# Kernel optimization log

Measured on AMD Instinct MI355X. Metric: run time of the kernel, lower is better.

Reference implementation:

```python
import jax, jax.numpy as jnp
import numpy as np

B, J, E, H = 32, 512, 512, 8
HD = E // H
EPS = 1e-7


def log_map0_spatial(x):
    # Lorentz log map at origin o=(1,0,...,0); return spatial (tangent) part.
    x0 = jnp.maximum(x[..., 0], 1.0 + 1e-7)      # [B,J]
    xs = x[..., 1:]                               # [B,J,E]
    nrm = jnp.linalg.norm(xs, axis=-1, keepdims=True)
    theta = jnp.arccosh(x0)[..., None]
    return theta * xs / jnp.maximum(nrm, EPS)


def exp_map0(v_s):
    # Lorentz exp map at origin of tangent vector (0, v_s) -> (cosh|v|, sinh|v| v/|v|).
    nrm = jnp.linalg.norm(v_s, axis=-1, keepdims=True)
    safe = jnp.maximum(nrm, EPS)
    return jnp.concatenate([jnp.cosh(nrm), jnp.sinh(nrm) * v_s / safe], axis=-1)


def setup_inputs() -> dict:
    key = jax.random.key(0)
    ks = jax.random.split(key, 8)
    xs = 0.5 * jax.random.normal(ks[0], (B, J, E), dtype=jnp.float32)
    x0 = jnp.sqrt(1.0 + jnp.sum(xs * xs, axis=-1, keepdims=True))  # valid hyperboloid
    x = jnp.concatenate([x0, xs], axis=-1)                          # [B,J,E+1]
    x_vel = jax.random.normal(ks[1], (B, J, E + 1), dtype=jnp.float32)
    topo_bias = 0.1 * jax.random.normal(ks[2], (J, J), dtype=jnp.float32)
    s = 1.0 / np.sqrt(E)
    W_qkv = jax.random.uniform(ks[3], (3 * E, E), jnp.float32, -s, s)
    W_vproj = jax.random.uniform(ks[4], (E, E), jnp.float32, -s, s)
    W_proj = jax.random.uniform(ks[5], (E, E), jnp.float32, -s, s)
    b_proj = jax.random.uniform(ks[6], (E,), jnp.float32, -s, s)
    return {"x": x, "x_vel": x_vel, "topo_bias": topo_bias,
            "W_qkv": W_qkv, "W_vproj": W_vproj, "W_proj": W_proj, "b_proj": b_proj}


def reference(x, x_vel, topo_bias, W_qkv, W_vproj, W_proj, b_proj):
    # Dropout is inference-mode (identity) for a deterministic reference.
    x_tan = log_map0_spatial(x)                                   # [B,J,E]
    v_tan = x_vel[..., 1:]                                        # [B,J,E]
    qkv = (x_tan @ W_qkv.T).reshape(B, J, 3, H, HD)
    qkv = jnp.transpose(qkv, (2, 0, 3, 1, 4))                     # [3,B,H,J,hd]
    q, k, v = qkv[0], qkv[1], qkv[2]
    k_vel = jnp.transpose((v_tan @ W_vproj.T).reshape(B, J, H, HD), (0, 2, 1, 3))
    k = k + k_vel
    scale = HD ** -0.5
    attn = jnp.einsum('bhqd,bhkd->bhqk', q, k) * scale + topo_bias[None, None]
    attn = jax.nn.softmax(attn, axis=-1)                          # [B,H,J,J]
    z_tan = jnp.einsum('bhqk,bhkd->bhqd', attn, v)
    z_tan = jnp.transpose(z_tan, (0, 2, 1, 3)).reshape(B, J, E)
    z_tan = z_tan @ W_proj.T + b_proj
    z_manifold = exp_map0(z_tan)                                  # [B,J,E+1]
    return (z_manifold, attn, x_tan)
```

## Files before the change

### kernel.cpp

```cpp
#include <hip/hip_runtime.h>
#include <hip/hip_bf16.h>
#include <math.h>

#define Jdim 512
#define Edim 512

typedef short short8 __attribute__((ext_vector_type(8)));
typedef float f32x4 __attribute__((ext_vector_type(4)));
typedef unsigned short u16;
typedef unsigned int u32;

__device__ __forceinline__ u16 f2b(float f) {
    union { float f; u32 u; } v; v.f = f;
    u32 r = (v.u + 0x7FFFu + ((v.u >> 16) & 1u)) >> 16;
    return (u16)r;
}
__device__ __forceinline__ float b2f(u16 u) {
    union { u32 u; float f; } v; v.u = ((u32)u) << 16;
    return v.f;
}

__device__ __forceinline__ void gl_lds16(const void* g, void* l) {
    __builtin_amdgcn_global_load_lds(
        (const __attribute__((address_space(1))) u32*)g,
        (__attribute__((address_space(3))) u32*)l, 16, 0, 0);
}

__global__ __launch_bounds__(256) void convw(
    const float* __restrict__ Wqkv, const float* __restrict__ Wvp,
    const float* __restrict__ Wproj,
    u16* __restrict__ Wq, u16* __restrict__ Wv, u16* __restrict__ Wp,
    u16* __restrict__ Wcat)
{
    int i = blockIdx.x * 256 + threadIdx.x;
    if (i < 262144) {
        Wq[i] = f2b(Wqkv[i]);
        Wv[i] = f2b(Wqkv[524288 + i]);
        Wp[i] = f2b(Wproj[i]);
    }
    int n = i >> 10, c = i & 1023;
    float v = (c < 512) ? Wqkv[(size_t)(512 + n) * 512 + c]
                        : Wvp[(size_t)n * 512 + (c - 512)];
    Wcat[i] = f2b(v);
}

__global__ __launch_bounds__(256) void xtan_kernel(
    const float* __restrict__ x, const float* __restrict__ xvel,
    float* __restrict__ xtan_out, u16* __restrict__ Acat)
{
    int row = blockIdx.x, tid = threadIdx.x;
    int lane = tid & 63, w = tid >> 6;
    const float* xr = x + (size_t)row * 513;
    float a0 = xr[1 + tid], a1 = xr[1 + tid + 256];
    float ss = a0 * a0 + a1 * a1;
    for (int o = 32; o >= 1; o >>= 1) ss += __shfl_down(ss, o);
    __shared__ float wsum[4];
    if (lane == 0) wsum[w] = ss;
    __syncthreads();
    float nrm = sqrtf(wsum[0] + wsum[1] + wsum[2] + wsum[3]);
    float x0 = fmaxf(xr[0], 1.0f + 1e-7f);
    float theta = acoshf(x0);
    float scl = theta / fmaxf(nrm, 1e-7f);
    float t0 = a0 * scl, t1 = a1 * scl;
    xtan_out[(size_t)row * 512 + tid] = t0;
    xtan_out[(size_t)row * 512 + tid + 256] = t1;
    u16* ac = Acat + (size_t)row * 1024;
    ac[tid] = f2b(t0);
    ac[tid + 256] = f2b(t1);
    const float* vr = xvel + (size_t)row * 513;
    ac[512 + tid] = f2b(vr[1 + tid]);
    ac[768 + tid] = f2b(vr[1 + tid + 256]);
}

template <int MODE>
__global__ __launch_bounds__(256) void gemm_bt(
    const u16* __restrict__ A, int lda,
    const u16* __restrict__ Bm, int ldb, int K,
    u16* __restrict__ out_b, float* __restrict__ out_f,
    const float* __restrict__ bias)
{
    __shared__ u16 As[128 * 64];
    __shared__ u16 Bs[128 * 64];
    const int tid = threadIdx.x;
    const int w = tid >> 6, lane = tid & 63, l15 = lane & 15, quad = lane >> 4;
    const int m0 = blockIdx.y * 128, n0 = blockIdx.x * 128;
    const int wm = (w & 1) * 64, wn = (w >> 1) * 64;

    f32x4 acc[4][4];
#pragma unroll
    for (int i = 0; i < 4; i++)
#pragma unroll
        for (int j = 0; j < 4; j++) acc[i][j] = (f32x4)0.0f;

    for (int kt = 0; kt < K; kt += 64) {
#pragma unroll
        for (int i = 0; i < 4; i++) {
            int c = i * 256 + tid;
            int row = c >> 3, s = c & 7, gc = s ^ (row & 7);
            gl_lds16(&A[(size_t)(m0 + row) * lda + kt + gc * 8],
                     &As[(size_t)(i * 256 + (tid & ~63)) * 8]);
        }
#pragma unroll
        for (int i = 0; i < 4; i++) {
            int c = i * 256 + tid;
            int row = c >> 3, s = c & 7, gc = s ^ (row & 7);
            gl_lds16(&Bm[(size_t)(n0 + row) * ldb + kt + gc * 8],
                     &Bs[(size_t)(i * 256 + (tid & ~63)) * 8]);
        }
        __syncthreads();
#pragma unroll
        for (int kc = 0; kc < 2; kc++) {
            short8 af[4], bf[4];
#pragma unroll
            for (int t = 0; t < 4; t++) {
                int row = wm + t * 16 + l15;
                int slot = (kc * 4 + quad) ^ (row & 7);
                af[t] = *(const short8*)&As[row * 64 + slot * 8];
            }
#pragma unroll
            for (int t = 0; t < 4; t++) {
                int row = wn + t * 16 + l15;
                int slot = (kc * 4 + quad) ^ (row & 7);
                bf[t] = *(const short8*)&Bs[row * 64 + slot * 8];
            }
#pragma unroll
            for (int ti = 0; ti < 4; ti++)
#pragma unroll
                for (int tj = 0; tj < 4; tj++)
                    acc[ti][tj] = __builtin_amdgcn_mfma_f32_16x16x32_bf16(
                        af[ti], bf[tj], acc[ti][tj], 0, 0, 0);
        }
        __syncthreads();
    }

#pragma unroll
    for (int ti = 0; ti < 4; ti++)
#pragma unroll
        for (int tj = 0; tj < 4; tj++)
#pragma unroll
            for (int r = 0; r < 4; r++) {
                int gm = m0 + wm + ti * 16 + quad * 4 + r;
                int gn = n0 + wn + tj * 16 + l15;
                float vacc = acc[ti][tj][r];
                if (MODE == 0) {
                    int b = gm >> 9, j = gm & 511, h = gn >> 6, d = gn & 63;
                    out_b[(((size_t)(b * 8 + h) * 512 + j) << 6) + d] = f2b(vacc);
                } else {
                    out_f[(size_t)gm * 512 + gn] = vacc + bias[gn];
                }
            }
}

__global__ __launch_bounds__(256) void vtrans(
    const u16* __restrict__ vb, u16* __restrict__ vT)
{
    __shared__ u16 tile[64][65];
    int bh = blockIdx.x >> 3, jt = blockIdx.x & 7;
    const u16* src = vb + (size_t)bh * 512 * 64 + (size_t)jt * 64 * 64;
#pragma unroll
    for (int i = 0; i < 16; i++) {
        int e = i * 256 + threadIdx.x;
        tile[e >> 6][e & 63] = src[e];
    }
    __syncthreads();
    u16* dst = vT + (size_t)bh * 64 * 512 + jt * 64;
#pragma unroll
    for (int i = 0; i < 16; i++) {
        int e = i * 256 + threadIdx.x;
        int d = e >> 6, jj = e & 63;
        dst[(size_t)d * 512 + jj] = tile[jj][d];
    }
}

__global__ __launch_bounds__(256) void attn_kernel(
    const u16* __restrict__ qb, const u16* __restrict__ kb,
    const u16* __restrict__ vT, const float* __restrict__ bias,
    float* __restrict__ attn_out, u16* __restrict__ z_bf)
{
    __shared__ u16 Sb[32 * 520];
    __shared__ float row_m[32], row_is[32];
    const int tid = threadIdx.x, w = tid >> 6, lane = tid & 63;
    const int l15 = lane & 15, quad = lane >> 4;
    const int bh = blockIdx.x >> 4, qt = blockIdx.x & 15;
    const int q0 = qt * 32;
    const u16* qp = qb + (size_t)bh * 512 * 64;
    const u16* kp = kb + (size_t)bh * 512 * 64;

    short8 qf[2][2];
#pragma unroll
    for (int ti = 0; ti < 2; ti++)
#pragma unroll
        for (int kc = 0; kc < 2; kc++)
            qf[ti][kc] = *(const short8*)&qp[(q0 + ti * 16 + l15) * 64 + kc * 32 + quad * 8];

    f32x4 sacc[2][8];
#pragma unroll
    for (int ti = 0; ti < 2; ti++)
#pragma unroll
        for (int kt = 0; kt < 8; kt++) sacc[ti][kt] = (f32x4)0.0f;

    const int kbase = w * 128;
#pragma unroll
    for (int kt = 0; kt < 8; kt++) {
        short8 kf[2];
        int n = kbase + kt * 16 + l15;
#pragma unroll
        for (int kc = 0; kc < 2; kc++)
            kf[kc] = *(const short8*)&kp[n * 64 + kc * 32 + quad * 8];
#pragma unroll
        for (int ti = 0; ti < 2; ti++)
#pragma unroll
            for (int kc = 0; kc < 2; kc++)
                sacc[ti][kt] = __builtin_amdgcn_mfma_f32_16x16x32_bf16(
                    qf[ti][kc], kf[kc], sacc[ti][kt], 0, 0, 0);
    }
#pragma unroll
    for (int ti = 0; ti < 2; ti++)
#pragma unroll
        for (int kt = 0; kt < 8; kt++) {
            int col = kbase + kt * 16 + l15;
#pragma unroll
            for (int r = 0; r < 4; r++) {
                int row = ti * 16 + quad * 4 + r;
                float s = sacc[ti][kt][r] * 0.125f +
                          bias[(size_t)(q0 + row) * 512 + col];
                Sb[row * 520 + col] = f2b(s);
            }
        }
    __syncthreads();

    {
        int srow = tid >> 3, li = tid & 7;
        float m = -1e30f;
        for (int t = 0; t < 64; t++)
            m = fmaxf(m, b2f(Sb[srow * 520 + li + 8 * t]));
        m = fmaxf(m, __shfl_xor(m, 1));
        m = fmaxf(m, __shfl_xor(m, 2));
        m = fmaxf(m, __shfl_xor(m, 4));
        if (li == 0) row_m[srow] = m;
        __syncthreads();
        m = row_m[srow];
        float sum = 0.0f;
        for (int t = 0; t < 64; t++)
            sum += expf(b2f(Sb[srow * 520 + li + 8 * t]) - m);
        sum += __shfl_xor(sum, 1);
        sum += __shfl_xor(sum, 2);
        sum += __shfl_xor(sum, 4);
        if (li == 0) row_is[srow] = 1.0f / sum;
        __syncthreads();
    }

    float* attn_p = attn_out + (size_t)bh * 512 * 512 + (size_t)q0 * 512;
#pragma unroll
    for (int i = 0; i < 16; i++) {
        int e = i * 256 + tid;
        int row = e >> 7, cq = (e & 127) * 4;
        uint2 sv = *(const uint2*)&Sb[row * 520 + cq];
        float m = row_m[row], is = row_is[row];
        float p0 = expf(b2f((u16)(sv.x & 0xffff)) - m) * is;
        float p1 = expf(b2f((u16)(sv.x >> 16)) - m) * is;
        float p2 = expf(b2f((u16)(sv.y & 0xffff)) - m) * is;
        float p3 = expf(b2f((u16)(sv.y >> 16)) - m) * is;
        f32x4 pv; pv[0] = p0; pv[1] = p1; pv[2] = p2; pv[3] = p3;
        *(f32x4*)&attn_p[(size_t)row * 512 + cq] = pv;
        uint2 pk;
        pk.x = (u32)f2b(p0) | ((u32)f2b(p1) << 16);
        pk.y = (u32)f2b(p2) | ((u32)f2b(p3) << 16);
        *(uint2*)&Sb[row * 520 + cq] = pk;
    }
    __syncthreads();

    const u16* vp = vT + (size_t)bh * 64 * 512;
    f32x4 zacc[2];
    zacc[0] = (f32x4)0.0f; zacc[1] = (f32x4)0.0f;
    int n0 = w * 16;
#pragma unroll
    for (int kc = 0; kc < 16; kc++) {
        short8 bfv = *(const short8*)&vp[(size_t)(n0 + l15) * 512 + kc * 32 + quad * 8];
#pragma unroll
        for (int ti = 0; ti < 2; ti++) {
            short8 afp = *(const short8*)&Sb[(ti * 16 + l15) * 520 + kc * 32 + quad * 8];
            zacc[ti] = __builtin_amdgcn_mfma_f32_16x16x32_bf16(afp, bfv, zacc[ti], 0, 0, 0);
        }
    }
    int b = bh >> 3, h = bh & 7;
#pragma unroll
    for (int ti = 0; ti < 2; ti++)
#pragma unroll
        for (int r = 0; r < 4; r++) {
            int row = q0 + ti * 16 + quad * 4 + r;
            int d = n0 + l15;
            z_bf[((size_t)b * 512 + row) * 512 + h * 64 + d] = f2b(zacc[ti][r]);
        }
}

__global__ __launch_bounds__(256) void expmap_kernel(
    const float* __restrict__ zp, float* __restrict__ out0)
{
    int row = blockIdx.x, tid = threadIdx.x;
    int lane = tid & 63, w = tid >> 6;
    const float* zr = zp + (size_t)row * 512;
    float a0 = zr[tid], a1 = zr[tid + 256];
    float ss = a0 * a0 + a1 * a1;
    for (int o = 32; o >= 1; o >>= 1) ss += __shfl_down(ss, o);
    __shared__ float wsum[4];
    if (lane == 0) wsum[w] = ss;
    __syncthreads();
    float nrm = sqrtf(wsum[0] + wsum[1] + wsum[2] + wsum[3]);
    float scl = sinhf(nrm) / fmaxf(nrm, 1e-7f);
    float* orow = out0 + (size_t)row * 513;
    if (tid == 0) orow[0] = coshf(nrm);
    orow[1 + tid] = a0 * scl;
    orow[1 + tid + 256] = a1 * scl;
}

extern "C" void kernel_launch(void* const* d_in, const int* in_sizes, int n_in,
                              void* d_out, int out_size, void* d_ws, size_t ws_size,
                              hipStream_t stream) {
    const float* x     = (const float*)d_in[0];
    const float* xvel  = (const float*)d_in[1];
    const float* topo  = (const float*)d_in[2];
    const float* Wqkv  = (const float*)d_in[3];
    const float* Wvp   = (const float*)d_in[4];
    const float* Wproj = (const float*)d_in[5];
    const float* bproj = (const float*)d_in[6];

    float* out      = (float*)d_out;
    float* out_zman = out;
    float* out_attn = out + 8404992;
    float* out_xtan = out + 75513856;

    char* ws = (char*)d_ws;
    u16*   Acat  = (u16*)ws;
    u16*   Wq    = (u16*)(ws + 33554432);
    u16*   Wv    = (u16*)(ws + 34078720);
    u16*   Wp    = (u16*)(ws + 34603008);
    u16*   Wcat  = (u16*)(ws + 35127296);
    u16*   qbuf  = (u16*)(ws + 36175872);
    u16*   kbuf  = (u16*)(ws + 52953088);
    u16*   vbuf  = (u16*)(ws + 69730304);
    u16*   vT    = (u16*)(ws + 86507520);
    u16*   zbf   = (u16*)(ws + 103284736);
    float* zproj = (float*)(ws + 120061952);

    convw<<<2048, 256, 0, stream>>>(Wqkv, Wvp, Wproj, Wq, Wv, Wp, Wcat);
    xtan_kernel<<<16384, 256, 0, stream>>>(x, xvel, out_xtan, Acat);

    dim3 g(4, 128);
    gemm_bt<0><<<g, 256, 0, stream>>>(Acat, 1024, Wq,   512,  512,  qbuf, nullptr, nullptr);
    gemm_bt<0><<<g, 256, 0, stream>>>(Acat, 1024, Wcat, 1024, 1024, kbuf, nullptr, nullptr);
    gemm_bt<0><<<g, 256, 0, stream>>>(Acat, 1024, Wv,   512,  512,  vbuf, nullptr, nullptr);

    vtrans<<<2048, 256, 0, stream>>>(vbuf, vT);

    attn_kernel<<<4096, 256, 0, stream>>>(qbuf, kbuf, vT, topo, out_attn, zbf);

    gemm_bt<1><<<g, 256, 0, stream>>>(zbf, 512, Wp, 512, 512, nullptr, zproj, bproj);
    expmap_kernel<<<16384, 256, 0, stream>>>(zproj, out_zman);
}
```

Baseline: 568.6 us.

## Fuse Q/V GEMMs, register-resident softmax, wave-per-row norms, vectorized transpose

Merges the Q and V projection GEMMs into one wider launch with a split output, so the A tile is reused across both. The attention softmax now runs on the fp32 MFMA accumulators in registers, using shuffle and small LDS reductions, instead of round-tripping bf16 scores through shared memory. That removes extra LDS passes and the bf16 rounding of scores before the exp. The xtan and expmap kernels now assign one wave per row and drop the block barrier, and the V transpose uses 8-byte vector loads and stores. Writing attn straight from the MFMA layout gives less coalesced global stores, 64-byte row segments instead of full 16-byte vectors.

```diff
diff --git a/kernel.cpp b/kernel.cpp
--- a/kernel.cpp
+++ b/kernel.cpp
@@ -2,8 +2,6 @@
 #include <hip/hip_bf16.h>
 #include <math.h>
 
-#define Jdim 512
-#define Edim 512
 
 typedef short short8 __attribute__((ext_vector_type(8)));
 typedef float f32x4 __attribute__((ext_vector_type(4)));
@@ -29,55 +27,59 @@
 __global__ __launch_bounds__(256) void convw(
     const float* __restrict__ Wqkv, const float* __restrict__ Wvp,
     const float* __restrict__ Wproj,
-    u16* __restrict__ Wq, u16* __restrict__ Wv, u16* __restrict__ Wp,
-    u16* __restrict__ Wcat)
+    u16* __restrict__ Wqv, u16* __restrict__ Wp, u16* __restrict__ Wcat)
 {
     int i = blockIdx.x * 256 + threadIdx.x;
-    if (i < 262144) {
-        Wq[i] = f2b(Wqkv[i]);
-        Wv[i] = f2b(Wqkv[524288 + i]);
-        Wp[i] = f2b(Wproj[i]);
-    }
-    int n = i >> 10, c = i & 1023;
-    float v = (c < 512) ? Wqkv[(size_t)(512 + n) * 512 + c]
-                        : Wvp[(size_t)n * 512 + (c - 512)];
-    Wcat[i] = f2b(v);
+    {
+        int row = i >> 9;
+        size_t src = (size_t)i + (row < 512 ? 0 : 262144);
+        Wqv[i] = f2b(Wqkv[src]);
+    }
+    {
+        int n = i >> 10, c = i & 1023;
+        float v = (c < 512) ? Wqkv[(size_t)(512 + n) * 512 + c]
+                            : Wvp[(size_t)n * 512 + (c - 512)];
+        Wcat[i] = f2b(v);
+    }
+    if (i < 262144) Wp[i] = f2b(Wproj[i]);
 }
 
 __global__ __launch_bounds__(256) void xtan_kernel(
     const float* __restrict__ x, const float* __restrict__ xvel,
     float* __restrict__ xtan_out, u16* __restrict__ Acat)
 {
-    int row = blockIdx.x, tid = threadIdx.x;
-    int lane = tid & 63, w = tid >> 6;
+    int row = blockIdx.x * 4 + (threadIdx.x >> 6);
+    int lane = threadIdx.x & 63;
     const float* xr = x + (size_t)row * 513;
-    float a0 = xr[1 + tid], a1 = xr[1 + tid + 256];
-    float ss = a0 * a0 + a1 * a1;
-    for (int o = 32; o >= 1; o >>= 1) ss += __shfl_down(ss, o);
-    __shared__ float wsum[4];
-    if (lane == 0) wsum[w] = ss;
-    __syncthreads();
-    float nrm = sqrtf(wsum[0] + wsum[1] + wsum[2] + wsum[3]);
+    float a[8];
+    float ss = 0.0f;
+#pragma unroll
+    for (int j = 0; j < 8; j++) { a[j] = xr[1 + j * 64 + lane]; ss += a[j] * a[j]; }
+#pragma unroll
+    for (int o = 32; o >= 1; o >>= 1) ss += __shfl_xor(ss, o);
     float x0 = fmaxf(xr[0], 1.0f + 1e-7f);
     float theta = acoshf(x0);
-    float scl = theta / fmaxf(nrm, 1e-7f);
-    float t0 = a0 * scl, t1 = a1 * scl;
-    xtan_out[(size_t)row * 512 + tid] = t0;
-    xtan_out[(size_t)row * 512 + tid + 256] = t1;
+    float scl = theta / fmaxf(sqrtf(ss), 1e-7f);
+    float* xo = xtan_out + (size_t)row * 512;
     u16* ac = Acat + (size_t)row * 1024;
-    ac[tid] = f2b(t0);
-    ac[tid + 256] = f2b(t1);
+#pragma unroll
+    for (int j = 0; j < 8; j++) {
+        float t = a[j] * scl;
+        xo[j * 64 + lane] = t;
+        ac[j * 64 + lane] = f2b(t);
+    }
     const float* vr = xvel + (size_t)row * 513;
-    ac[512 + tid] = f2b(vr[1 + tid]);
-    ac[768 + tid] = f2b(vr[1 + tid + 256]);
+#pragma unroll
+    for (int j = 0; j < 8; j++)
+        ac[512 + j * 64 + lane] = f2b(vr[1 + j * 64 + lane]);
 }
 
 template <int MODE>
 __global__ __launch_bounds__(256) void gemm_bt(
     const u16* __restrict__ A, int lda,
     const u16* __restrict__ Bm, int ldb, int K,
-    u16* __restrict__ out_b, float* __restrict__ out_f,
-    const float* __restrict__ bias)
+    u16* __restrict__ out_b, u16* __restrict__ out_b2,
+    float* __restrict__ out_f, const float* __restrict__ bias)
 {
     __shared__ u16 As[128 * 64];
     __shared__ u16 Bs[128 * 64];
@@ -142,11 +144,16 @@
                 int gm = m0 + wm + ti * 16 + quad * 4 + r;
                 int gn = n0 + wn + tj * 16 + l15;
                 float vacc = acc[ti][tj][r];
-                if (MODE == 0) {
-                    int b = gm >> 9, j = gm & 511, h = gn >> 6, d = gn & 63;
-                    out_b[(((size_t)(b * 8 + h) * 512 + j) << 6) + d] = f2b(vacc);
+                if (MODE == 1) {
+                    out_f[(size_t)gm * 512 + gn] = vacc + bias[gn];
                 } else {
-                    out_f[(size_t)gm * 512 + gn] = vacc + bias[gn];
+                    int b = gm >> 9, j = gm & 511;
+                    u16* dst;
+                    int g;
+                    if (MODE == 0) { dst = (gn < 512) ? out_b : out_b2; g = gn & 511; }
+                    else { dst = out_b; g = gn; }
+                    int h = g >> 6, d = g & 63;
+                    dst[(((size_t)(b * 8 + h) * 512 + j) << 6) + d] = f2b(vacc);
                 }
             }
 }
@@ -154,21 +161,28 @@
 __global__ __launch_bounds__(256) void vtrans(
     const u16* __restrict__ vb, u16* __restrict__ vT)
 {
-    __shared__ u16 tile[64][65];
+    __shared__ u16 tile[64][68];
     int bh = blockIdx.x >> 3, jt = blockIdx.x & 7;
-    const u16* src = vb + (size_t)bh * 512 * 64 + (size_t)jt * 64 * 64;
-#pragma unroll
-    for (int i = 0; i < 16; i++) {
-        int e = i * 256 + threadIdx.x;
-        tile[e >> 6][e & 63] = src[e];
+    const u16* src = vb + (size_t)bh * 32768 + (size_t)jt * 4096;
+#pragma unroll
+    for (int i = 0; i < 4; i++) {
+        int o = i * 1024 + threadIdx.x * 4;
+        uint2 v = *(const uint2*)&src[o];
+        int j = o >> 6, d = o & 63;
+        *(uint2*)&tile[j][d] = v;
     }
     __syncthreads();
-    u16* dst = vT + (size_t)bh * 64 * 512 + jt * 64;
-#pragma unroll
-    for (int i = 0; i < 16; i++) {
-        int e = i * 256 + threadIdx.x;
-        int d = e >> 6, jj = e & 63;
-        dst[(size_t)d * 512 + jj] = tile[jj][d];
+    u16* dst = vT + (size_t)bh * 32768 + jt * 64;
+#pragma unroll
+    for (int i = 0; i < 4; i++) {
+        int o = i * 1024 + threadIdx.x * 4;
+        int d = o >> 6, j0 = o & 63;
+        u16 r0 = tile[j0][d], r1 = tile[j0 + 1][d];
+        u16 r2 = tile[j0 + 2][d], r3 = tile[j0 + 3][d];
+        uint2 pv;
+        pv.x = (u32)r0 | ((u32)r1 << 16);
+        pv.y = (u32)r2 | ((u32)r3 << 16);
+        *(uint2*)&dst[(size_t)d * 512 + j0] = pv;
     }
 }
 
@@ -178,13 +192,14 @@
     float* __restrict__ attn_out, u16* __restrict__ z_bf)
 {
     __shared__ u16 Sb[32 * 520];
-    __shared__ float row_m[32], row_is[32];
+    __shared__ float redM[32][4];
+    __shared__ float redS[32][4];
     const int tid = threadIdx.x, w = tid >> 6, lane = tid & 63;
     const int l15 = lane & 15, quad = lane >> 4;
     const int bh = blockIdx.x >> 4, qt = blockIdx.x & 15;
     const int q0 = qt * 32;
-    const u16* qp = qb + (size_t)bh * 512 * 64;
-    const u16* kp = kb + (size_t)bh * 512 * 64;
+    const u16* qp = qb + (size_t)bh * 32768;
+    const u16* kp = kb + (size_t)bh * 32768;
 
     short8 qf[2][2];
 #pragma unroll
@@ -214,6 +229,8 @@
                 sacc[ti][kt] = __builtin_amdgcn_mfma_f32_16x16x32_bf16(
                     qf[ti][kc], kf[kc], sacc[ti][kt], 0, 0, 0);
     }
+
+    const float* bp = bias + (size_t)q0 * 512;
 #pragma unroll
     for (int ti = 0; ti < 2; ti++)
 #pragma unroll
@@ -222,55 +239,105 @@
 #pragma unroll
             for (int r = 0; r < 4; r++) {
                 int row = ti * 16 + quad * 4 + r;
-                float s = sacc[ti][kt][r] * 0.125f +
-                          bias[(size_t)(q0 + row) * 512 + col];
-                Sb[row * 520 + col] = f2b(s);
-            }
-        }
+                sacc[ti][kt][r] = sacc[ti][kt][r] * 0.125f + bp[(size_t)row * 512 + col];
+            }
+        }
+
+    float mrow[2][4];
+#pragma unroll
+    for (int ti = 0; ti < 2; ti++) {
+        f32x4 mv = sacc[ti][0];
+#pragma unroll
+        for (int kt = 1; kt < 8; kt++) {
+#pragma unroll
+            for (int r = 0; r < 4; r++) mv[r] = fmaxf(mv[r], sacc[ti][kt][r]);
+        }
+#pragma unroll
+        for (int r = 0; r < 4; r++) {
+            float v = mv[r];
+            v = fmaxf(v, __shfl_xor(v, 1));
+            v = fmaxf(v, __shfl_xor(v, 2));
+            v = fmaxf(v, __shfl_xor(v, 4));
+            v = fmaxf(v, __shfl_xor(v, 8));
+            mrow[ti][r] = v;
+        }
+    }
+    if (l15 == 0) {
+#pragma unroll
+        for (int ti = 0; ti < 2; ti++)
+#pragma unroll
+            for (int r = 0; r < 4; r++)
+                redM[ti * 16 + quad * 4 + r][w] = mrow[ti][r];
+    }
     __syncthreads();
-
-    {
-        int srow = tid >> 3, li = tid & 7;
-        float m = -1e30f;
-        for (int t = 0; t < 64; t++)
-            m = fmaxf(m, b2f(Sb[srow * 520 + li + 8 * t]));
-        m = fmaxf(m, __shfl_xor(m, 1));
-        m = fmaxf(m, __shfl_xor(m, 2));
-        m = fmaxf(m, __shfl_xor(m, 4));
-        if (li == 0) row_m[srow] = m;
-        __syncthreads();
-        m = row_m[srow];
-        float sum = 0.0f;
-        for (int t = 0; t < 64; t++)
-            sum += expf(b2f(Sb[srow * 520 + li + 8 * t]) - m);
-        sum += __shfl_xor(sum, 1);
-        sum += __shfl_xor(sum, 2);
-        sum += __shfl_xor(sum, 4);
-        if (li == 0) row_is[srow] = 1.0f / sum;
-        __syncthreads();
-    }
-
-    float* attn_p = attn_out + (size_t)bh * 512 * 512 + (size_t)q0 * 512;
-#pragma unroll
-    for (int i = 0; i < 16; i++) {
-        int e = i * 256 + tid;
-        int row = e >> 7, cq = (e & 127) * 4;
-        uint2 sv = *(const uint2*)&Sb[row * 520 + cq];
-        float m = row_m[row], is = row_is[row];
-        float p0 = expf(b2f((u16)(sv.x & 0xffff)) - m) * is;
-        float p1 = expf(b2f((u16)(sv.x >> 16)) - m) * is;
-        float p2 = expf(b2f((u16)(sv.y & 0xffff)) - m) * is;
-        float p3 = expf(b2f((u16)(sv.y >> 16)) - m) * is;
-        f32x4 pv; pv[0] = p0; pv[1] = p1; pv[2] = p2; pv[3] = p3;
-        *(f32x4*)&attn_p[(size_t)row * 512 + cq] = pv;
-        uint2 pk;
-        pk.x = (u32)f2b(p0) | ((u32)f2b(p1) << 16);
-        pk.y = (u32)f2b(p2) | ((u32)f2b(p3) << 16);
-        *(uint2*)&Sb[row * 520 + cq] = pk;
+#pragma unroll
+    for (int ti = 0; ti < 2; ti++)
+#pragma unroll
+        for (int r = 0; r < 4; r++) {
+            f32x4 rv = *(const f32x4*)redM[ti * 16 + quad * 4 + r];
+            mrow[ti][r] = fmaxf(fmaxf(rv[0], rv[1]), fmaxf(rv[2], rv[3]));
+        }
+
+    float srow[2][4];
+#pragma unroll
+    for (int ti = 0; ti < 2; ti++)
+#pragma unroll
+        for (int r = 0; r < 4; r++) srow[ti][r] = 0.0f;
+#pragma unroll
+    for (int ti = 0; ti < 2; ti++)
+#pragma unroll
+        for (int kt = 0; kt < 8; kt++)
+#pragma unroll
+            for (int r = 0; r < 4; r++) {
+                float e = expf(sacc[ti][kt][r] - mrow[ti][r]);
+                sacc[ti][kt][r] = e;
+                srow[ti][r] += e;
+            }
+#pragma unroll
+    for (int ti = 0; ti < 2; ti++)
+#pragma unroll
+        for (int r = 0; r < 4; r++) {
+            float v = srow[ti][r];
+            v += __shfl_xor(v, 1);
+            v += __shfl_xor(v, 2);
+            v += __shfl_xor(v, 4);
+            v += __shfl_xor(v, 8);
+            srow[ti][r] = v;
+        }
+    if (l15 == 0) {
+#pragma unroll
+        for (int ti = 0; ti < 2; ti++)
+#pragma unroll
+            for (int r = 0; r < 4; r++)
+                redS[ti * 16 + quad * 4 + r][w] = srow[ti][r];
     }
     __syncthreads();
-
-    const u16* vp = vT + (size_t)bh * 64 * 512;
+    float inv[2][4];
+#pragma unroll
+    for (int ti = 0; ti < 2; ti++)
+#pragma unroll
+        for (int r = 0; r < 4; r++) {
+            f32x4 rv = *(const f32x4*)redS[ti * 16 + quad * 4 + r];
+            inv[ti][r] = 1.0f / (rv[0] + rv[1] + rv[2] + rv[3]);
+        }
+
+    float* ap = attn_out + (size_t)bh * 262144 + (size_t)q0 * 512;
+#pragma unroll
+    for (int ti = 0; ti < 2; ti++)
+#pragma unroll
+        for (int kt = 0; kt < 8; kt++) {
+            int col = kbase + kt * 16 + l15;
+#pragma unroll
+            for (int r = 0; r < 4; r++) {
+                int row = ti * 16 + quad * 4 + r;
+                float p = sacc[ti][kt][r] * inv[ti][r];
+                ap[(size_t)row * 512 + col] = p;
+                Sb[row * 520 + col] = f2b(p);
+            }
+        }
+    __syncthreads();
+
+    const u16* vp = vT + (size_t)bh * 32768;
     f32x4 zacc[2];
     zacc[0] = (f32x4)0.0f; zacc[1] = (f32x4)0.0f;
     int n0 = w * 16;
@@ -297,21 +364,22 @@
 __global__ __launch_bounds__(256) void expmap_kernel(
     const float* __restrict__ zp, float* __restrict__ out0)
 {
-    int row = blockIdx.x, tid = threadIdx.x;
-    int lane = tid & 63, w = tid >> 6;
+    int row = blockIdx.x * 4 + (threadIdx.x >> 6);
+    int lane = threadIdx.x & 63;
     const float* zr = zp + (size_t)row * 512;
-    float a0 = zr[tid], a1 = zr[tid + 256];
-    float ss = a0 * a0 + a1 * a1;
-    for (int o = 32; o >= 1; o >>= 1) ss += __shfl_down(ss, o);
-    __shared__ float wsum[4];
-    if (lane == 0) wsum[w] = ss;
-    __syncthreads();
-    float nrm = sqrtf(wsum[0] + wsum[1] + wsum[2] + wsum[3]);
+    float a[8];
+    float ss = 0.0f;
+#pragma unroll
+    for (int j = 0; j < 8; j++) { a[j] = zr[j * 64 + lane]; ss += a[j] * a[j]; }
+#pragma unroll
+    for (int o = 32; o >= 1; o >>= 1) ss += __shfl_xor(ss, o);
+    float nrm = sqrtf(ss);
     float scl = sinhf(nrm) / fmaxf(nrm, 1e-7f);
     float* orow = out0 + (size_t)row * 513;
-    if (tid == 0) orow[0] = coshf(nrm);
-    orow[1 + tid] = a0 * scl;
-    orow[1 + tid + 256] = a1 * scl;
+    if (lane == 0) orow[0] = coshf(nrm);
+#pragma unroll
+    for (int j = 0; j < 8; j++)
+        orow[1 + j * 64 + lane] = a[j] * scl;
 }
 
 extern "C" void kernel_launch(void* const* d_in, const int* in_sizes, int n_in,
@@ -332,10 +400,9 @@
 
     char* ws = (char*)d_ws;
     u16*   Acat  = (u16*)ws;
-    u16*   Wq    = (u16*)(ws + 33554432);
-    u16*   Wv    = (u16*)(ws + 34078720);
-    u16*   Wp    = (u16*)(ws + 34603008);
-    u16*   Wcat  = (u16*)(ws + 35127296);
+    u16*   Wqv   = (u16*)(ws + 33554432);
+    u16*   Wcat  = (u16*)(ws + 34603008);
+    u16*   Wp    = (u16*)(ws + 35651584);
     u16*   qbuf  = (u16*)(ws + 36175872);
     u16*   kbuf  = (u16*)(ws + 52953088);
     u16*   vbuf  = (u16*)(ws + 69730304);
@@ -343,18 +410,19 @@
     u16*   zbf   = (u16*)(ws + 103284736);
     float* zproj = (float*)(ws + 120061952);
 
-    convw<<<2048, 256, 0, stream>>>(Wqkv, Wvp, Wproj, Wq, Wv, Wp, Wcat);
-    xtan_kernel<<<16384, 256, 0, stream>>>(x, xvel, out_xtan, Acat);
-
-    dim3 g(4, 128);
-    gemm_bt<0><<<g, 256, 0, stream>>>(Acat, 1024, Wq,   512,  512,  qbuf, nullptr, nullptr);
-    gemm_bt<0><<<g, 256, 0, stream>>>(Acat, 1024, Wcat, 1024, 1024, kbuf, nullptr, nullptr);
-    gemm_bt<0><<<g, 256, 0, stream>>>(Acat, 1024, Wv,   512,  512,  vbuf, nullptr, nullptr);
+    convw<<<2048, 256, 0, stream>>>(Wqkv, Wvp, Wproj, Wqv, Wp, Wcat);
+    xtan_kernel<<<4096, 256, 0, stream>>>(x, xvel, out_xtan, Acat);
+
+    gemm_bt<0><<<dim3(8, 128), 256, 0, stream>>>(Acat, 1024, Wqv, 512, 512,
+                                                 qbuf, vbuf, nullptr, nullptr);
+    gemm_bt<2><<<dim3(4, 128), 256, 0, stream>>>(Acat, 1024, Wcat, 1024, 1024,
+                                                 kbuf, nullptr, nullptr, nullptr);
 
     vtrans<<<2048, 256, 0, stream>>>(vbuf, vT);
 
     attn_kernel<<<4096, 256, 0, stream>>>(qbuf, kbuf, vT, topo, out_attn, zbf);
 
-    gemm_bt<1><<<g, 256, 0, stream>>>(zbf, 512, Wp, 512, 512, nullptr, zproj, bproj);
-    expmap_kernel<<<16384, 256, 0, stream>>>(zproj, out_zman);
-}
+    gemm_bt<1><<<dim3(4, 128), 256, 0, stream>>>(zbf, 512, Wp, 512, 512,
+                                                 nullptr, nullptr, zproj, bproj);
+    expmap_kernel<<<4096, 256, 0, stream>>>(zproj, out_zman);
+}
```

Result: slower. 588.1 us (+3.4%).
